# Kernel tuning notes

Measured on AMD Instinct MI355X. Metric: run time of the kernel, lower is better.

Reference implementation:

```python
import jax, jax.numpy as jnp
import numpy as np
from jax import lax

# dims
B, N, K = 8, 1024, 32          # batch, nodes, kNN neighbors
D, H, DH = 256, 8, 32           # node feature width, heads, head dim
TDIM, NB, HID = 16, 32, 128     # time-embed dim, radial basis count, radial MLP hidden
NLAYERS = 3                     # hidden transformer layers
L = NLAYERS + 1                 # + output layer
NS = 128                        # scalar channels sliced into edge attrs
SHD = 9                         # spherical harmonics dim for lmax=2 (1+3+5)
RMAX = 2.0
EIN = NB + TDIM + 2 * NS        # edge-MLP input width


def _sph(u):
    # real spherical harmonics l=0,1,2 with 'component' normalization of unit vec u
    x, y, z = u[..., 0], u[..., 1], u[..., 2]
    l0 = jnp.ones_like(x)[..., None]
    l1 = np.sqrt(3.0) * u
    l2 = jnp.stack([
        np.sqrt(15.0) * x * y,
        np.sqrt(15.0) * y * z,
        0.5 * np.sqrt(5.0) * (3.0 * z * z - 1.0),
        np.sqrt(15.0) * x * z,
        0.5 * np.sqrt(15.0) * (x * x - y * y),
    ], -1)
    return jnp.concatenate([l0, l1, l2], -1)


def _rbf(r):
    # e3nn soft_one_hot_linspace(basis='gaussian', cutoff=False) * sqrt(NB) * 0.95
    centers = jnp.linspace(0.0, RMAX, NB)
    step = RMAX / (NB - 1)
    e = jnp.exp(-((r[..., None] - centers) / step) ** 2) / 1.12
    return e * (NB ** 0.5) * 0.95


def _sus(x):
    # e3nn smooth unit step: exp(-1/x) for x>0 else 0
    return jnp.where(x > 0, jnp.exp(-1.0 / jnp.where(x > 0, x, 1.0)), 0.0)


def setup_inputs() -> dict:
    key = jax.random.key(0)
    ks = jax.random.split(key, 12)
    g = lambda k, shape, fan: (jax.random.normal(k, shape, jnp.float32) / np.sqrt(fan))
    return {
        'x': jax.random.normal(ks[0], (B, N, 3), jnp.float32),
        'y': jax.random.normal(ks[1], (B, N, 3), jnp.float32),
        't': jax.random.uniform(ks[2], (B, TDIM), jnp.float32),
        'W_embed': g(ks[3], (3 + TDIM, D), 3 + TDIM),
        'Wk1': g(ks[4], (L, EIN, HID), EIN),
        'bk1': jnp.zeros((L, HID), jnp.float32),
        'Wk2': g(ks[5], (L, HID, H * DH), HID),
        'Wq': g(ks[6], (L, D, H * DH), D),
        'Wv': g(ks[7], (L, D + SHD, H * DH), D + SHD),
        'Wo': g(ks[8], (NLAYERS, H * DH, D), H * DH),
        'Wo_out': g(ks[9], (H * DH, 3), H * DH),
    }


def _forward(x, y, t, W_embed, Wk1, bk1, Wk2, Wq, Wv, Wo, Wo_out):
    def score(pos, feat, tt):
        # kNN graph: full pairwise distance + top_k (self included, as in source)
        d2 = jnp.sum((pos[:, None, :] - pos[None, :, :]) ** 2, -1)      # [N,N]
        src = lax.top_k(-d2, K)[1]                                       # [N,K], dst = row index
        vec = pos[:, None, :] - pos[src]                                 # pos[dst]-pos[src], [N,K,3]
        r = jnp.linalg.norm(vec, axis=-1)                                # [N,K]
        u = vec / jnp.maximum(r[..., None], 1e-9)
        sh = _sph(u)                                                     # [N,K,SHD]
        cut = 1.4 * _sus(10.0 * (1.0 - r / RMAX))                        # [N,K]
        rbf = _rbf(r) * cut[..., None]                                   # [N,K,NB]
        t_nodes = jnp.broadcast_to(tt, (N, TDIM))
        edge_base = jnp.concatenate([rbf, jnp.broadcast_to(tt, (N, K, TDIM))], -1)
        node = jnp.concatenate([feat, t_nodes], -1) @ W_embed            # [N,D]
        for l in range(L):
            # gather scalar node channels onto edges
            e = jnp.concatenate([edge_base, node[src][..., :NS],
                                 jnp.broadcast_to(node[:, None, :NS], (N, K, NS))], -1)  # [N,K,EIN]
            h = jax.nn.gelu(e @ Wk1[l] + bk1[l])                          # radial MLP
            kf = (h @ Wk2[l]).reshape(N, K, H, DH)
            q = (node @ Wq[l]).reshape(N, H, DH)
            logits = jnp.einsum('nhd,nkhd->nkh', q, kf) / np.sqrt(DH)
            # cutoff-weighted softmax over neighbors (e3nn Transformer style)
            w = cut[..., None] * jnp.exp(logits - logits.max(1, keepdims=True))
            alpha = w / (w.sum(1, keepdims=True) + 1e-9)                  # [N,K,H]
            v = (jnp.concatenate([node[src], sh], -1) @ Wv[l]).reshape(N, K, H, DH)
            agg = jnp.einsum('nkh,nkhd->nhd', alpha, v).reshape(N, H * DH)
            if l < NLAYERS:
                node = node + agg @ Wo[l]                                  # residual
                # scalar activation: gelu on 0e, tanh on 0o, identity on higher l
                node = jnp.concatenate([jax.nn.gelu(node[:, :64]),
                                        jnp.tanh(node[:, 64:NS]),
                                        node[:, NS:]], -1)
            else:
                node = agg @ Wo_out                                        # project to 1x1e
        return node  # [N,3]

    return jax.vmap(score)(x, y, t)


def reference(x, y, t, W_embed, Wk1, bk1, Wk2, Wq, Wv, Wo, Wo_out):
    return _forward(x, y, t, W_embed, Wk1, bk1, Wk2, Wq, Wv, Wo, Wo_out)
```

## Files before the change

kernel.cpp:

```cpp
#include <hip/hip_runtime.h>
#include <math.h>

#define Bb 8
#define Nn 1024
#define Kk 32
#define Dd 256
#define Hh 8
#define DHh 32
#define TDIMt 16
#define NBnb 32
#define HIDh 128
#define NSns 128
#define SHDs 9
#define EINe 304
#define NCOLS 1536

typedef __bf16 bf16_t;
typedef bf16_t bf16x8 __attribute__((ext_vector_type(8)));
typedef float floatx4 __attribute__((ext_vector_type(4)));

#define GLOAD_LDS16(gp, lp) __builtin_amdgcn_global_load_lds( \
    (const __attribute__((address_space(1))) void*)(gp),      \
    (__attribute__((address_space(3))) void*)(lp), 16, 0, 0)

__device__ __forceinline__ float gelu_fast(float x){
  float g = 1.5957691216057308f*(x + 0.044715f*x*x*x);
  return x*__builtin_amdgcn_rcpf(1.0f + __expf(-g));
}
__device__ __forceinline__ float tanh_fast(float x){
  return 1.0f - 2.0f*__builtin_amdgcn_rcpf(1.0f + __expf(2.0f*x));
}

__global__ __launch_bounds__(256) void setup_kernel(
    const float* __restrict__ x, const float* __restrict__ y, const float* __restrict__ t,
    const float* __restrict__ We, const float* __restrict__ Wk1, const float* __restrict__ bk1,
    const float* __restrict__ Wk2, const float* __restrict__ Wq, const float* __restrict__ Wv,
    const float* __restrict__ Wo,
    bf16_t* __restrict__ Wt, bf16_t* __restrict__ Wto, bf16_t* __restrict__ WrbfT,
    float* __restrict__ t_hd, int* __restrict__ src,
    float* __restrict__ node, bf16_t* __restrict__ node_bf){

  __shared__ float s_b[32];
  __shared__ unsigned long long s_knn[4][64];
  const int bid = blockIdx.x, tid = threadIdx.x;

  if (bid < 2048){
    int wave = tid >> 6, lane = tid & 63;
    int bn = bid*4 + wave;
    int b = bn >> 10, n = bn & (Nn-1);
    const float* xb = x + (size_t)b*Nn*3;
    float px = xb[n*3+0], py = xb[n*3+1], pz = xb[n*3+2];
    float d2v[16];
    #pragma unroll
    for (int i=0;i<16;i++){
      int j = i*64 + lane;
      float dx = px - xb[j*3+0];
      float dy = py - xb[j*3+1];
      float dz = pz - xb[j*3+2];
      d2v[i] = dx*dx + dy*dy + dz*dz;
    }

    unsigned lob = 0u, hib = 0x7149F2CAu;
    float T = 1.0f;
    int lc = 0;
    for (int it=0; it<24; ++it){
      lc = 0;
      #pragma unroll
      for (int i=0;i<16;i++) lc += (d2v[i] <= T) ? 1 : 0;
      int c = lc;
      #pragma unroll
      for (int off=32; off>=1; off>>=1) c += __shfl_xor(c, off);
      if (c >= 32 && c <= 64) break;
      if (c < 32) lob = __float_as_uint(T); else hib = __float_as_uint(T);
      float ratio = 44.0f * __builtin_amdgcn_rcpf((float)(c < 1 ? 1 : c));
      float Tn = T * __powf(ratio, 0.6666667f);
      unsigned tb = __float_as_uint(Tn);
      if (tb <= lob || tb >= hib) tb = lob + ((hib - lob) >> 1);
      T = __uint_as_float(tb);
    }

    int pre = lc;
    #pragma unroll
    for (int d=1; d<64; d<<=1){
      int o = __shfl_up(pre, d);
      if (lane >= d) pre += o;
    }
    int wo = pre - lc;

    unsigned long long* sl = s_knn[wave];
    sl[lane] = ~0ull;
    #pragma unroll
    for (int i=0;i<16;i++){
      if (d2v[i] <= T && wo < 64){
        sl[wo] = (((unsigned long long)__float_as_uint(d2v[i])) << 10)
                 | (unsigned)(i*64 + lane);
        wo++;
      }
    }
    __syncthreads();

    unsigned long long key = sl[lane];
    #pragma unroll
    for (int k2=2; k2<=64; k2<<=1){
      #pragma unroll
      for (int j2=k2>>1; j2>=1; j2>>=1){
        unsigned long long pv = __shfl_xor(key, j2);
        bool takeMin = (((lane & j2) == 0) == ((lane & k2) == 0));
        bool pLess = pv < key;
        key = (pLess == takeMin) ? pv : key;
      }
    }
    if (lane < 32) src[(size_t)bn*Kk + lane] = (int)(key & 1023u);
  } else if (bid < 6144){
    int i = bid-2048; int l = i>>10, yy = i&1023;
    int h = yy>>7, c = yy&127;
    if (tid < 32) s_b[tid] = Wk2[(size_t)l*HIDh*Dd + (size_t)c*Dd + h*DHh + tid];
    __syncthreads();
    const int rloc = tid>>3, dg = tid&7;
    const float b0 = s_b[dg*4+0], b1 = s_b[dg*4+1], b2 = s_b[dg*4+2], b3 = s_b[dg*4+3];
    #pragma unroll
    for (int p=0;p<8;p++){
      int ii = p*32 + rloc;
      const float4 v = *(const float4*)(Wq + (size_t)l*Dd*Dd + (size_t)ii*Dd + h*DHh + dg*4);
      float part = v.x*b0 + v.y*b1 + v.z*b2 + v.w*b3;
      part += __shfl_xor(part, 1);
      part += __shfl_xor(part, 2);
      part += __shfl_xor(part, 4);
      if (dg == 0) Wt[((size_t)l*NCOLS + 512 + yy)*Dd + ii] = (bf16_t)part;
    }
  } else if (bid < 8192){
    int i = bid-6144; int l = i>>9, c = i&511, k = tid;
    const float* wk1l = Wk1 + (size_t)l*EINe*HIDh;
    float v;
    if (c < 256)       v = Wv[(size_t)l*265*Dd + (size_t)k*Dd + c];
    else if (c < 384){ int c2 = c-256; v = (k < 128) ? wk1l[(48+k)*HIDh + c2] : 0.0f; }
    else             { int c2 = c-384; v = (k < 128) ? wk1l[(176+k)*HIDh + c2] : 0.0f; }
    Wt[((size_t)l*NCOLS + c)*Dd + k] = (bf16_t)v;
  } else if (bid < 8960){
    int i = bid-8192; int l = i>>8; int c = i&255; int k = tid;
    Wto[((size_t)l*Dd + c)*Dd + k] = (bf16_t)Wo[(size_t)l*Dd*Dd + (size_t)k*Dd + c];
  } else if (bid < 9024){
    int i = bid-8960; int l = i>>4, cg = i&15;
    int c = cg*8 + (tid>>5), k = tid&31;
    WrbfT[((size_t)l*HIDh + c)*NBnb + k] = (bf16_t)Wk1[(size_t)l*EINe*HIDh + (size_t)k*HIDh + c];
  } else if (bid < 9040){
    int i = bid-9024; int pair = i*2 + (tid>>7);
    int l = pair>>3, b = pair&7, c = tid&127;
    const float* wk1l = Wk1 + (size_t)l*EINe*HIDh;
    float a = bk1[l*HIDh + c];
    #pragma unroll
    for (int ii=0;ii<TDIMt;ii++) a += t[b*TDIMt+ii]*wk1l[(32+ii)*HIDh + c];
    t_hd[(l*Bb + b)*HIDh + c] = a;
  } else {
    int bn0 = (bid-9040)*4; int c = tid;
    float w0 = We[0*Dd+c], w1 = We[1*Dd+c], w2 = We[2*Dd+c];
    float wt[TDIMt];
    #pragma unroll
    for (int i=0;i<TDIMt;i++) wt[i] = We[(3+i)*Dd+c];
    #pragma unroll
    for (int u=0;u<4;u++){
      int bn = bn0 + u; int b = bn >> 10;
      float a = y[(size_t)bn*3+0]*w0 + y[(size_t)bn*3+1]*w1 + y[(size_t)bn*3+2]*w2;
      #pragma unroll
      for (int i=0;i<TDIMt;i++) a += t[b*TDIMt+i]*wt[i];
      node[(size_t)bn*Dd + c] = a;
      node_bf[(size_t)bn*Dd + c] = (bf16_t)a;
    }
  }
}

__global__ __launch_bounds__(256) void gemm_proj(const bf16_t* __restrict__ A,
    const bf16_t* __restrict__ Wt_all, float* __restrict__ vproj_f,
    bf16_t* __restrict__ hsrc_bf, float* __restrict__ hdst_f,
    bf16_t* __restrict__ qw_bf, const float* __restrict__ t_hd, int layer){

  __shared__ __align__(16) bf16_t s_A[2][8192];
  __shared__ __align__(16) bf16_t s_B[2][4096];

  const int tid = threadIdx.x;
  const int wave = tid>>6, lane = tid&63;
  const int row16 = lane&15, quad = lane>>4;
  const int bx = blockIdx.x;
  const int brow = ((bx & 7) << 3) + (bx >> 3);
  const int m0 = brow*128;
  const int m_base = m0 + wave*32;
  const int n_base = blockIdx.y*64;
  const bf16_t* Ab = A + (size_t)m0*Dd;
  const bf16_t* Bw = Wt_all + ((size_t)layer*NCOLS + n_base)*Dd;

  const int trow = tid>>3;
  const int tk   = ((tid&7) ^ (trow&7)) << 3;
  const int swz  = (row16&7) << 3;

  floatx4 acc[2][4];
  #pragma unroll
  for (int mi=0;mi<2;mi++)
    #pragma unroll
    for (int ni=0;ni<4;ni++){ floatx4 z = {0.f,0.f,0.f,0.f}; acc[mi][ni] = z; }

  {
    const bf16_t* ga = Ab + (size_t)trow*Dd + tk;
    #pragma unroll
    for (int i=0;i<4;i++) GLOAD_LDS16(ga + (size_t)i*32*Dd, &s_A[0][i*2048 + tid*8]);
    const bf16_t* gb = Bw + (size_t)trow*Dd + tk;
    #pragma unroll
    for (int j=0;j<2;j++) GLOAD_LDS16(gb + (size_t)j*32*Dd, &s_B[0][j*2048 + tid*8]);
  }
  __syncthreads();

  #pragma unroll
  for (int kt=0; kt<4; kt++){
    const int cur = kt&1, nxt = cur^1;
    if (kt < 3){
      const bf16_t* ga = Ab + (size_t)trow*Dd + (kt+1)*64 + tk;
      #pragma unroll
      for (int i=0;i<4;i++) GLOAD_LDS16(ga + (size_t)i*32*Dd, &s_A[nxt][i*2048 + tid*8]);
      const bf16_t* gb = Bw + (size_t)trow*Dd + (kt+1)*64 + tk;
      #pragma unroll
      for (int j=0;j<2;j++) GLOAD_LDS16(gb + (size_t)j*32*Dd, &s_B[nxt][j*2048 + tid*8]);
    }
    #pragma unroll
    for (int ksub=0; ksub<2; ksub++){
      const int ko = (ksub*32 + quad*8) ^ swz;
      bf16x8 a0 = *(const bf16x8*)&s_A[cur][(wave*32      + row16)*64 + ko];
      bf16x8 a1 = *(const bf16x8*)&s_A[cur][(wave*32 + 16 + row16)*64 + ko];
      #pragma unroll
      for (int ni=0;ni<4;ni++){
        bf16x8 b = *(const bf16x8*)&s_B[cur][(ni*16 + row16)*64 + ko];
        acc[0][ni] = __builtin_amdgcn_mfma_f32_16x16x32_bf16(a0, b, acc[0][ni], 0,0,0);
        acc[1][ni] = __builtin_amdgcn_mfma_f32_16x16x32_bf16(a1, b, acc[1][ni], 0,0,0);
      }
    }
    __syncthreads();
  }

  const int by = blockIdx.y;
  const int bb = m_base >> 10;
  #pragma unroll
  for (int mi=0;mi<2;mi++)
    #pragma unroll
    for (int ni=0;ni<4;ni++){
      int col = n_base + ni*16 + row16;
      #pragma unroll
      for (int r=0;r<4;r++){
        int row = m_base + mi*16 + quad*4 + r;
        float v = acc[mi][ni][r];
        if (by < 4)       vproj_f[(size_t)row*256 + col]        = v;
        else if (by < 6)  hsrc_bf[(size_t)row*128 + (col-256)]  = (bf16_t)v;
        else if (by < 8)  hdst_f[(size_t)row*128 + (col-384)]   = v + t_hd[(size_t)(layer*Bb + bb)*HIDh + (col-384)];
        else              qw_bf[(size_t)row*1024 + (col-512)]   = (bf16_t)v;
      }
    }
}

__global__ __launch_bounds__(256) void gemm_upd(
    const bf16_t* __restrict__ agg_bf, const bf16_t* __restrict__ Wto,
    const float* __restrict__ node_in, float* __restrict__ node_out,
    bf16_t* __restrict__ node_bf, int lu, int write_node){

  __shared__ __align__(16) bf16_t s_A[2][8192];
  __shared__ __align__(16) bf16_t s_B[2][4096];

  const int tid = threadIdx.x;
  const int wave = tid>>6, lane = tid&63;
  const int row16 = lane&15, quad = lane>>4;
  const int bx = blockIdx.x;
  const int brow = ((bx & 7) << 3) + (bx >> 3);
  const int m0 = brow*128;
  const int m_base = m0 + wave*32;
  const int n_base = blockIdx.y*64;
  const bf16_t* Ab = agg_bf + (size_t)m0*Dd;
  const bf16_t* Bw = Wto + (size_t)lu*Dd*Dd + (size_t)n_base*Dd;

  const int trow = tid>>3;
  const int tk   = ((tid&7) ^ (trow&7)) << 3;
  const int swz  = (row16&7) << 3;

  floatx4 acc[2][4];
  #pragma unroll
  for (int mi=0;mi<2;mi++)
    #pragma unroll
    for (int ni=0;ni<4;ni++){ floatx4 z = {0.f,0.f,0.f,0.f}; acc[mi][ni] = z; }

  {
    const bf16_t* ga = Ab + (size_t)trow*Dd + tk;
    #pragma unroll
    for (int i=0;i<4;i++) GLOAD_LDS16(ga + (size_t)i*32*Dd, &s_A[0][i*2048 + tid*8]);
    const bf16_t* gb = Bw + (size_t)trow*Dd + tk;
    #pragma unroll
    for (int j=0;j<2;j++) GLOAD_LDS16(gb + (size_t)j*32*Dd, &s_B[0][j*2048 + tid*8]);
  }
  __syncthreads();

  #pragma unroll
  for (int kt=0; kt<4; kt++){
    const int cur = kt&1, nxt = cur^1;
    if (kt < 3){
      const bf16_t* ga = Ab + (size_t)trow*Dd + (kt+1)*64 + tk;
      #pragma unroll
      for (int i=0;i<4;i++) GLOAD_LDS16(ga + (size_t)i*32*Dd, &s_A[nxt][i*2048 + tid*8]);
      const bf16_t* gb = Bw + (size_t)trow*Dd + (kt+1)*64 + tk;
      #pragma unroll
      for (int j=0;j<2;j++) GLOAD_LDS16(gb + (size_t)j*32*Dd, &s_B[nxt][j*2048 + tid*8]);
    }
    #pragma unroll
    for (int ksub=0; ksub<2; ksub++){
      const int ko = (ksub*32 + quad*8) ^ swz;
      bf16x8 a0 = *(const bf16x8*)&s_A[cur][(wave*32      + row16)*64 + ko];
      bf16x8 a1 = *(const bf16x8*)&s_A[cur][(wave*32 + 16 + row16)*64 + ko];
      #pragma unroll
      for (int ni=0;ni<4;ni++){
        bf16x8 b = *(const bf16x8*)&s_B[cur][(ni*16 + row16)*64 + ko];
        acc[0][ni] = __builtin_amdgcn_mfma_f32_16x16x32_bf16(a0, b, acc[0][ni], 0,0,0);
        acc[1][ni] = __builtin_amdgcn_mfma_f32_16x16x32_bf16(a1, b, acc[1][ni], 0,0,0);
      }
    }
    __syncthreads();
  }

  #pragma unroll
  for (int mi=0;mi<2;mi++)
    #pragma unroll
    for (int ni=0;ni<4;ni++){
      int col = n_base + ni*16 + row16;
      #pragma unroll
      for (int r=0;r<4;r++){
        int row = m_base + mi*16 + quad*4 + r;
        float v = acc[mi][ni][r] + node_in[(size_t)row*Dd + col];
        if (col < 64)       v = gelu_fast(v);
        else if (col < 128) v = tanh_fast(v);
        if (write_node) node_out[(size_t)row*Dd + col] = v;
        node_bf[(size_t)row*Dd + col] = (bf16_t)v;
      }
    }
}

__global__ __launch_bounds__(128) void attn_kernel(
    const float* __restrict__ x, const int* __restrict__ src,
    const float* __restrict__ vproj_f, const bf16_t* __restrict__ hsrc_bf,
    const float* __restrict__ hdst_f, const bf16_t* __restrict__ qw_bf,
    const bf16_t* __restrict__ WrbfT,
    const float* __restrict__ Wvg, const float* __restrict__ Woo,
    bf16_t* __restrict__ agg_bf, float* __restrict__ out, int layer){

  __shared__ __align__(16) char smem[11488];
  bf16_t* s_h     = (bf16_t*)(smem);
  float*  s_part  = (float*)(smem);
  float*  s_sh    = (float*)(smem + 8704);
  float*  s_cut   = (float*)(smem + 9984);
  float*  s_logit = (float*)(smem + 10112);
  float*  s_pool  = (float*)(smem + 11136);
  float*  s_red   = (float*)(smem + 11456);

  const int tid  = threadIdx.x;
  const int bidx = blockIdx.x;
  const int b    = bidx & 7;
  const int bn   = (b << 10) | (bidx >> 3);
  const int wv   = tid>>6, lane = tid&63;
  const int row16 = lane&15, quad = lane>>4;

  bf16x8 qf[4];
  { const bf16_t* qp = qw_bf + (size_t)bn*1024 + row16*HIDh + quad*8;
    #pragma unroll
    for (int ks=0; ks<4; ks++) qf[ks] = *(const bf16x8*)(qp + ks*32); }
  float hdv[4];
  #pragma unroll
  for (int ni=0; ni<4; ni++) hdv[ni] = hdst_f[(size_t)bn*128 + wv*64 + ni*16 + row16];

  const float ax = x[(size_t)bn*3+0], ay = x[(size_t)bn*3+1], az = x[(size_t)bn*3+2];

  const int sE0 = src[(size_t)bn*Kk + row16];
  const int sE1 = src[(size_t)bn*Kk + row16 + 16];

  const int e0 = tid>>3, cg = tid&7;
  const int sG0 = src[(size_t)bn*Kk + e0];
  const int sG1 = src[(size_t)bn*Kk + e0 + 16];
  bf16x8 hsv00 = *(const bf16x8*)(hsrc_bf + ((size_t)b*Nn + sG0)*128 + cg*8);
  bf16x8 hsv01 = *(const bf16x8*)(hsrc_bf + ((size_t)b*Nn + sG0)*128 + cg*8 + 64);
  bf16x8 hsv10 = *(const bf16x8*)(hsrc_bf + ((size_t)b*Nn + sG1)*128 + cg*8);
  bf16x8 hsv11 = *(const bf16x8*)(hsrc_bf + ((size_t)b*Nn + sG1)*128 + cg*8 + 64);

  bf16x8 a0f, a1f;
  {
    const float* xj0 = x + ((size_t)b*Nn + sE0)*3;
    const float* xj1 = x + ((size_t)b*Nn + sE1)*3;
    float d0x = ax - xj0[0], d0y = ay - xj0[1], d0z = az - xj0[2];
    float d1x = ax - xj1[0], d1y = ay - xj1[1], d1z = az - xj1[2];
    float rr0 = sqrtf(d0x*d0x + d0y*d0y + d0z*d0z);
    float rr1 = sqrtf(d1x*d1x + d1y*d1y + d1z*d1z);
    float xx0 = 10.0f*(1.0f - rr0*0.5f);
    float xx1 = 10.0f*(1.0f - rr1*0.5f);
    float cu0 = (xx0 > 0.0f) ? 1.4f*__expf(-__builtin_amdgcn_rcpf(xx0)) : 0.0f;
    float cu1 = (xx1 > 0.0f) ? 1.4f*__expf(-__builtin_amdgcn_rcpf(xx1)) : 0.0f;
    float sc0 = 4.798224586623f*cu0;
    float sc1 = 4.798224586623f*cu1;
    float rs0 = fminf(rr0*15.5f, 33.0f);
    float rs1 = fminf(rr1*15.5f, 33.0f);
    float cbase = (float)(quad*8);
    float dd0 = rs0 - cbase, dd1 = rs1 - cbase;
    float e0v = __expf(-dd0*dd0)*sc0;
    float e1v = __expf(-dd1*dd1)*sc1;
    float g0 = __expf(2.0f*dd0 - 1.0f);
    float g1 = __expf(2.0f*dd1 - 1.0f);
    a0f[0] = (bf16_t)e0v; a1f[0] = (bf16_t)e1v;
    #pragma unroll
    for (int j=1;j<8;j++){
      e0v *= g0; e1v *= g1;
      a0f[j] = (bf16_t)e0v; a1f[j] = (bf16_t)e1v;
      g0 *= 0.13533528323661270f; g1 *= 0.13533528323661270f;
    }
  }

  if (tid < 64){
    const int k = tid & 31;
    const int j = src[(size_t)bn*Kk + k];
    const float* xj = x + ((size_t)b*Nn + j)*3;
    float dx = ax - xj[0], dy = ay - xj[1], dz = az - xj[2];
    float rr = sqrtf(dx*dx + dy*dy + dz*dz);
    if (tid < 32){
      float xx = 10.0f*(1.0f - rr*0.5f);
      s_cut[k] = (xx > 0.0f) ? 1.4f*__expf(-__builtin_amdgcn_rcpf(xx)) : 0.0f;
    } else {
      float inv = __builtin_amdgcn_rcpf(fmaxf(rr, 1e-9f));
      float ux = dx*inv, uy = dy*inv, uz = dz*inv;
      float* sh = s_sh + k*10;
      sh[0] = 1.0f;
      sh[1] = 1.7320508075688772f*ux;
      sh[2] = 1.7320508075688772f*uy;
      sh[3] = 1.7320508075688772f*uz;
      sh[4] = 3.872983346207417f*ux*uy;
      sh[5] = 3.872983346207417f*uy*uz;
      sh[6] = 1.118033988749895f*(3.0f*uz*uz - 1.0f);
      sh[7] = 3.872983346207417f*ux*uz;
      sh[8] = 1.9364916731037085f*(ux*ux - uy*uy);
    }
  }

  floatx4 acc[2][4];
  {
    #pragma unroll
    for (int mi=0;mi<2;mi++)
      #pragma unroll
      for (int ni=0;ni<4;ni++){ floatx4 z = {0.f,0.f,0.f,0.f}; acc[mi][ni] = z; }
    const bf16_t* bp = WrbfT + ((size_t)layer*HIDh + wv*64 + row16)*NBnb + quad*8;
    #pragma unroll
    for (int j=0;j<4;j++){
      bf16x8 bbf = *(const bf16x8*)(bp + (size_t)j*16*NBnb);
      acc[0][j] = __builtin_amdgcn_mfma_f32_16x16x32_bf16(a0f, bbf, acc[0][j], 0,0,0);
      acc[1][j] = __builtin_amdgcn_mfma_f32_16x16x32_bf16(a1f, bbf, acc[1][j], 0,0,0);
    }
  }

  *(bf16x8*)(s_h + e0*136 + cg*8)            = hsv00;
  *(bf16x8*)(s_h + e0*136 + cg*8 + 64)       = hsv01;
  *(bf16x8*)(s_h + (e0+16)*136 + cg*8)       = hsv10;
  *(bf16x8*)(s_h + (e0+16)*136 + cg*8 + 64)  = hsv11;
  __syncthreads();

  #pragma unroll
  for (int ni=0;ni<4;ni++){
    int c = wv*64 + ni*16 + row16;
    #pragma unroll
    for (int mi=0;mi<2;mi++){
      #pragma unroll
      for (int r=0;r<4;r++){
        int e = mi*16 + quad*4 + r;
        float hs = (float)s_h[e*136 + c];
        s_h[e*136 + c] = (bf16_t)gelu_fast(acc[mi][ni][r] + hdv[ni] + hs);
      }
    }
  }
  __syncthreads();

  {
    floatx4 la = {0.f,0.f,0.f,0.f};
    #pragma unroll
    for (int ks=0; ks<4; ks++){
      bf16x8 a = *(const bf16x8*)(s_h + (wv*16 + row16)*136 + ks*32 + quad*8);
      la = __builtin_amdgcn_mfma_f32_16x16x32_bf16(a, qf[ks], la, 0,0,0);
    }
    if (row16 < Hh){
      #pragma unroll
      for (int r=0;r<4;r++)
        s_logit[(wv*16 + quad*4 + r)*8 + row16] = la[r]*0.17677669529663687f;
    }
  }
  __syncthreads();

  {
    const int k = tid & 31;
    const int h0 = tid >> 5;
    #pragma unroll
    for (int hh=0; hh<2; hh++){
      const int h = h0 + hh*4;
      float lv = s_logit[k*8 + h];
      float m = lv;
      #pragma unroll
      for (int off=16; off>=1; off>>=1) m = fmaxf(m, __shfl_xor(m, off));
      float w = s_cut[k]*__expf(lv - m);
      float ss = w;
      #pragma unroll
      for (int off=16; off>=1; off>>=1) ss += __shfl_xor(ss, off);
      s_logit[k*8 + h] = w*__builtin_amdgcn_rcpf(ss + 1e-9f);
    }
  }
  __syncthreads();

  {
    const int h2 = tid>>4, sg = tid&15;
    if (sg < SHDs){
      float a = 0.0f;
      #pragma unroll
      for (int k2=0;k2<Kk;k2++)
        a += s_logit[k2*8 + h2] * s_sh[k2*10 + sg];
      s_pool[h2*10 + sg] = a;
    }
  }

  {
    const float* rowp[16];
    #pragma unroll
    for (int i=0;i<16;i++){
      int row = __builtin_amdgcn_readfirstlane(src[(size_t)bn*Kk + wv*16 + i]);
      rowp[i] = vproj_f + ((size_t)b*Nn + row)*256;
    }
    const int albase = wv*128 + (lane>>3);
    float4 accv = {0.f,0.f,0.f,0.f};
    #pragma unroll
    for (int i=0;i<16;i++){
      const float4 v = *(const float4*)(rowp[i] + (lane<<2));
      float al = s_logit[albase + i*8];
      accv.x += al*v.x; accv.y += al*v.y; accv.z += al*v.z; accv.w += al*v.w;
    }
    *(float4*)(s_part + wv*256 + (lane<<2)) = accv;
  }
  __syncthreads();

  {
    const float* wvsh = Wvg + (size_t)layer*265*Dd + 256*Dd;
    float p0 = 0.f, p1 = 0.f, p2 = 0.f;
    #pragma unroll
    for (int cc=0; cc<2; cc++){
      const int c = tid + cc*128;
      const int h = c >> 5;
      float a_main = s_part[c] + s_part[256 + c];
      #pragma unroll
      for (int sg=0; sg<SHDs; sg++) a_main += s_pool[h*10 + sg]*wvsh[sg*Dd + c];

      if (layer < 3){
        agg_bf[(size_t)bn*Dd + c] = (bf16_t)a_main;
      } else {
        p0 += a_main*Woo[c*3+0];
        p1 += a_main*Woo[c*3+1];
        p2 += a_main*Woo[c*3+2];
      }
    }
    if (layer >= 3){
      #pragma unroll
      for (int off=32; off>=1; off>>=1){
        p0 += __shfl_xor(p0, off);
        p1 += __shfl_xor(p1, off);
        p2 += __shfl_xor(p2, off);
      }
      if (lane == 0){ s_red[wv*3+0]=p0; s_red[wv*3+1]=p1; s_red[wv*3+2]=p2; }
      __syncthreads();
      if (tid < 3)
        out[(size_t)bn*3 + tid] = s_red[tid] + s_red[3+tid];
    }
  }
}

extern "C" void kernel_launch(void* const* d_in, const int* in_sizes, int n_in,
                              void* d_out, int out_size, void* d_ws, size_t ws_size,
                              hipStream_t stream){
  const float* x   = (const float*)d_in[0];
  const float* y   = (const float*)d_in[1];
  const float* t   = (const float*)d_in[2];
  const float* We  = (const float*)d_in[3];
  const float* Wk1 = (const float*)d_in[4];
  const float* bk1 = (const float*)d_in[5];
  const float* Wk2 = (const float*)d_in[6];
  const float* Wq  = (const float*)d_in[7];
  const float* Wv  = (const float*)d_in[8];
  const float* Wo  = (const float*)d_in[9];
  const float* Woo = (const float*)d_in[10];
  float* out = (float*)d_out;

  char* ws = (char*)d_ws;
  size_t off = 0;
  auto take = [&](size_t bytes)->char*{ char* p = ws + off; off = (off + bytes + 255) & ~(size_t)255; return p; };

  int*    src      = (int*)   take((size_t)Bb*Nn*Kk*4);
  float*  nodeA    = (float*) take((size_t)Bb*Nn*Dd*4);
  float*  nodeB    = (float*) take((size_t)Bb*Nn*Dd*4);
  bf16_t* node_bf  = (bf16_t*)take((size_t)Bb*Nn*Dd*2);
  bf16_t* agg_bf   = (bf16_t*)take((size_t)Bb*Nn*Dd*2);
  float*  vproj_f  = (float*) take((size_t)Bb*Nn*256*4);
  bf16_t* hsrc_bf  = (bf16_t*)take((size_t)Bb*Nn*128*2);
  float*  hdst_f   = (float*) take((size_t)Bb*Nn*128*4);
  bf16_t* qw_bf    = (bf16_t*)take(((size_t)Bb*Nn*1024 + 2048)*2);
  bf16_t* Wt       = (bf16_t*)take((size_t)4*NCOLS*Dd*2);
  bf16_t* Wto      = (bf16_t*)take((size_t)3*Dd*Dd*2);
  bf16_t* WrbfT    = (bf16_t*)take((size_t)4*HIDh*NBnb*2);
  float*  t_hd     = (float*) take((size_t)4*Bb*HIDh*4);

  setup_kernel<<<dim3(11088), 256, 0, stream>>>(x, y, t, We, Wk1, bk1, Wk2, Wq, Wv, Wo,
                                                Wt, Wto, WrbfT, t_hd, src, nodeA, node_bf);

  gemm_proj<<<dim3(64,24), 256, 0, stream>>>(node_bf, Wt, vproj_f, hsrc_bf, hdst_f, qw_bf, t_hd, 0);
  attn_kernel<<<dim3(Bb*Nn), 128, 0, stream>>>(x, src, vproj_f, hsrc_bf, hdst_f, qw_bf,
                                               WrbfT, Wv, Woo, agg_bf, out, 0);
  const float* nin[3]  = {nodeA, nodeB, nodeA};
  float*       nout[3] = {nodeB, nodeA, nodeB};
  for (int l=1; l<4; l++){
    gemm_upd<<<dim3(64,4), 256, 0, stream>>>(agg_bf, Wto, nin[l-1], nout[l-1], node_bf,
                                             l-1, (l < 3) ? 1 : 0);
    gemm_proj<<<dim3(64,24), 256, 0, stream>>>(node_bf, Wt, vproj_f, hsrc_bf, hdst_f, qw_bf, t_hd, l);
    attn_kernel<<<dim3(Bb*Nn), 128, 0, stream>>>(x, src, vproj_f, hsrc_bf, hdst_f, qw_bf,
                                                 WrbfT, Wv, Woo, agg_bf, out, l);
  }
}
```

Measured before the change: 399.0 us.

## Restructure attention kernel to one wave per node, four nodes per block

```diff
diff --git a/kernel.cpp b/kernel.cpp
--- a/kernel.cpp
+++ b/kernel.cpp
@@ -17,6 +17,7 @@
 
 typedef __bf16 bf16_t;
 typedef bf16_t bf16x8 __attribute__((ext_vector_type(8)));
+typedef bf16_t bf16x4v __attribute__((ext_vector_type(4)));
 typedef float floatx4 __attribute__((ext_vector_type(4)));
 
 #define GLOAD_LDS16(gp, lp) __builtin_amdgcn_global_load_lds( \
@@ -335,7 +336,7 @@
     }
 }
 
-__global__ __launch_bounds__(128) void attn_kernel(
+__global__ __launch_bounds__(256) void attn_kernel(
     const float* __restrict__ x, const int* __restrict__ src,
     const float* __restrict__ vproj_f, const bf16_t* __restrict__ hsrc_bf,
     const float* __restrict__ hdst_f, const bf16_t* __restrict__ qw_bf,
@@ -343,43 +344,42 @@
     const float* __restrict__ Wvg, const float* __restrict__ Woo,
     bf16_t* __restrict__ agg_bf, float* __restrict__ out, int layer){
 
-  __shared__ __align__(16) char smem[11488];
-  bf16_t* s_h     = (bf16_t*)(smem);
-  float*  s_part  = (float*)(smem);
-  float*  s_sh    = (float*)(smem + 8704);
-  float*  s_cut   = (float*)(smem + 9984);
-  float*  s_logit = (float*)(smem + 10112);
-  float*  s_pool  = (float*)(smem + 11136);
-  float*  s_red   = (float*)(smem + 11456);
-
+  __shared__ __align__(16) char smem[46080];
   const int tid  = threadIdx.x;
+  const int wave = tid>>6, lane = tid&63;
+  char* sw = smem + wave*11520;
+  bf16_t* s_h   = (bf16_t*)(sw);
+  float*  s_al  = (float*)(sw + 8704);
+  float*  s_sh  = (float*)(sw + 9728);
+  float*  s_cut = (float*)(sw + 11008);
+  float*  s_pool= (float*)(sw + 11136);
+
   const int bidx = blockIdx.x;
   const int b    = bidx & 7;
-  const int bn   = (b << 10) | (bidx >> 3);
-  const int wv   = tid>>6, lane = tid&63;
+  const int bn   = (b << 10) | ((bidx >> 3) << 2) | wave;
   const int row16 = lane&15, quad = lane>>4;
 
   bf16x8 qf[4];
   { const bf16_t* qp = qw_bf + (size_t)bn*1024 + row16*HIDh + quad*8;
     #pragma unroll
     for (int ks=0; ks<4; ks++) qf[ks] = *(const bf16x8*)(qp + ks*32); }
-  float hdv[4];
-  #pragma unroll
-  for (int ni=0; ni<4; ni++) hdv[ni] = hdst_f[(size_t)bn*128 + wv*64 + ni*16 + row16];
+  float hdv[8];
+  #pragma unroll
+  for (int j=0; j<8; j++) hdv[j] = hdst_f[(size_t)bn*128 + j*16 + row16];
 
   const float ax = x[(size_t)bn*3+0], ay = x[(size_t)bn*3+1], az = x[(size_t)bn*3+2];
+
+  bf16x8 hsv[8];
+  {
+    const int eg = lane>>1, half = lane&1;
+    const int sG = src[(size_t)bn*Kk + eg];
+    const bf16_t* hp = hsrc_bf + ((size_t)b*Nn + sG)*128 + half*64;
+    #pragma unroll
+    for (int j=0;j<8;j++) hsv[j] = *(const bf16x8*)(hp + j*8);
+  }
 
   const int sE0 = src[(size_t)bn*Kk + row16];
   const int sE1 = src[(size_t)bn*Kk + row16 + 16];
-
-  const int e0 = tid>>3, cg = tid&7;
-  const int sG0 = src[(size_t)bn*Kk + e0];
-  const int sG1 = src[(size_t)bn*Kk + e0 + 16];
-  bf16x8 hsv00 = *(const bf16x8*)(hsrc_bf + ((size_t)b*Nn + sG0)*128 + cg*8);
-  bf16x8 hsv01 = *(const bf16x8*)(hsrc_bf + ((size_t)b*Nn + sG0)*128 + cg*8 + 64);
-  bf16x8 hsv10 = *(const bf16x8*)(hsrc_bf + ((size_t)b*Nn + sG1)*128 + cg*8);
-  bf16x8 hsv11 = *(const bf16x8*)(hsrc_bf + ((size_t)b*Nn + sG1)*128 + cg*8 + 64);
-
   bf16x8 a0f, a1f;
   {
     const float* xj0 = x + ((size_t)b*Nn + sE0)*3;
@@ -411,13 +411,13 @@
     }
   }
 
-  if (tid < 64){
-    const int k = tid & 31;
+  {
+    const int k = lane & 31;
     const int j = src[(size_t)bn*Kk + k];
     const float* xj = x + ((size_t)b*Nn + j)*3;
     float dx = ax - xj[0], dy = ay - xj[1], dz = az - xj[2];
     float rr = sqrtf(dx*dx + dy*dy + dz*dz);
-    if (tid < 32){
+    if (lane < 32){
       float xx = 10.0f*(1.0f - rr*0.5f);
       s_cut[k] = (xx > 0.0f) ? 1.4f*__expf(-__builtin_amdgcn_rcpf(xx)) : 0.0f;
     } else {
@@ -436,136 +436,151 @@
     }
   }
 
-  floatx4 acc[2][4];
-  {
-    #pragma unroll
-    for (int mi=0;mi<2;mi++)
-      #pragma unroll
-      for (int ni=0;ni<4;ni++){ floatx4 z = {0.f,0.f,0.f,0.f}; acc[mi][ni] = z; }
-    const bf16_t* bp = WrbfT + ((size_t)layer*HIDh + wv*64 + row16)*NBnb + quad*8;
-    #pragma unroll
-    for (int j=0;j<4;j++){
+  floatx4 acc0[8], acc1[8];
+  {
+    const bf16_t* bp = WrbfT + ((size_t)layer*HIDh + row16)*NBnb + quad*8;
+    #pragma unroll
+    for (int j=0;j<8;j++){
+      floatx4 z = {0.f,0.f,0.f,0.f};
       bf16x8 bbf = *(const bf16x8*)(bp + (size_t)j*16*NBnb);
-      acc[0][j] = __builtin_amdgcn_mfma_f32_16x16x32_bf16(a0f, bbf, acc[0][j], 0,0,0);
-      acc[1][j] = __builtin_amdgcn_mfma_f32_16x16x32_bf16(a1f, bbf, acc[1][j], 0,0,0);
-    }
-  }
-
-  *(bf16x8*)(s_h + e0*136 + cg*8)            = hsv00;
-  *(bf16x8*)(s_h + e0*136 + cg*8 + 64)       = hsv01;
-  *(bf16x8*)(s_h + (e0+16)*136 + cg*8)       = hsv10;
-  *(bf16x8*)(s_h + (e0+16)*136 + cg*8 + 64)  = hsv11;
-  __syncthreads();
-
-  #pragma unroll
-  for (int ni=0;ni<4;ni++){
-    int c = wv*64 + ni*16 + row16;
-    #pragma unroll
-    for (int mi=0;mi<2;mi++){
+      acc0[j] = __builtin_amdgcn_mfma_f32_16x16x32_bf16(a0f, bbf, z, 0,0,0);
+      acc1[j] = __builtin_amdgcn_mfma_f32_16x16x32_bf16(a1f, bbf, z, 0,0,0);
+    }
+  }
+
+  {
+    const int eg = lane>>1, half = lane&1;
+    #pragma unroll
+    for (int j=0;j<8;j++)
+      *(bf16x8*)(s_h + eg*136 + half*64 + j*8) = hsv[j];
+  }
+
+  #pragma unroll
+  for (int j=0;j<8;j++){
+    const int c = j*16 + row16;
+    const float hd = hdv[j];
+    #pragma unroll
+    for (int r=0;r<4;r++){
+      int e = quad*4 + r;
+      float hs = (float)s_h[e*136 + c];
+      s_h[e*136 + c] = (bf16_t)gelu_fast(acc0[j][r] + hd + hs);
+    }
+    #pragma unroll
+    for (int r=0;r<4;r++){
+      int e = 16 + quad*4 + r;
+      float hs = (float)s_h[e*136 + c];
+      s_h[e*136 + c] = (bf16_t)gelu_fast(acc1[j][r] + hd + hs);
+    }
+  }
+
+  floatx4 la[2];
+  #pragma unroll
+  for (int rg=0; rg<2; rg++){
+    floatx4 l4 = {0.f,0.f,0.f,0.f};
+    #pragma unroll
+    for (int ks=0; ks<4; ks++){
+      bf16x8 a = *(const bf16x8*)(s_h + (rg*16 + row16)*136 + ks*32 + quad*8);
+      l4 = __builtin_amdgcn_mfma_f32_16x16x32_bf16(a, qf[ks], l4, 0,0,0);
+    }
+    la[rg] = l4;
+  }
+
+  {
+    float lv[8], ct[8];
+    #pragma unroll
+    for (int rg=0; rg<2; rg++)
       #pragma unroll
       for (int r=0;r<4;r++){
-        int e = mi*16 + quad*4 + r;
-        float hs = (float)s_h[e*136 + c];
-        s_h[e*136 + c] = (bf16_t)gelu_fast(acc[mi][ni][r] + hdv[ni] + hs);
-      }
-    }
-  }
-  __syncthreads();
-
-  {
-    floatx4 la = {0.f,0.f,0.f,0.f};
-    #pragma unroll
-    for (int ks=0; ks<4; ks++){
-      bf16x8 a = *(const bf16x8*)(s_h + (wv*16 + row16)*136 + ks*32 + quad*8);
-      la = __builtin_amdgcn_mfma_f32_16x16x32_bf16(a, qf[ks], la, 0,0,0);
-    }
+        lv[rg*4+r] = la[rg][r]*0.17677669529663687f;
+        ct[rg*4+r] = s_cut[rg*16 + quad*4 + r];
+      }
+    float m = lv[0];
+    #pragma unroll
+    for (int i=1;i<8;i++) m = fmaxf(m, lv[i]);
+    m = fmaxf(m, __shfl_xor(m, 16));
+    m = fmaxf(m, __shfl_xor(m, 32));
+    float w[8]; float ss = 0.f;
+    #pragma unroll
+    for (int i=0;i<8;i++){ w[i] = ct[i]*__expf(lv[i]-m); ss += w[i]; }
+    ss += __shfl_xor(ss, 16);
+    ss += __shfl_xor(ss, 32);
+    float rs = __builtin_amdgcn_rcpf(ss + 1e-9f);
     if (row16 < Hh){
       #pragma unroll
-      for (int r=0;r<4;r++)
-        s_logit[(wv*16 + quad*4 + r)*8 + row16] = la[r]*0.17677669529663687f;
-    }
-  }
-  __syncthreads();
-
-  {
-    const int k = tid & 31;
-    const int h0 = tid >> 5;
-    #pragma unroll
-    for (int hh=0; hh<2; hh++){
-      const int h = h0 + hh*4;
-      float lv = s_logit[k*8 + h];
-      float m = lv;
-      #pragma unroll
-      for (int off=16; off>=1; off>>=1) m = fmaxf(m, __shfl_xor(m, off));
-      float w = s_cut[k]*__expf(lv - m);
-      float ss = w;
-      #pragma unroll
-      for (int off=16; off>=1; off>>=1) ss += __shfl_xor(ss, off);
-      s_logit[k*8 + h] = w*__builtin_amdgcn_rcpf(ss + 1e-9f);
-    }
-  }
-  __syncthreads();
-
-  {
-    const int h2 = tid>>4, sg = tid&15;
-    if (sg < SHDs){
-      float a = 0.0f;
+      for (int rg=0; rg<2; rg++)
+        #pragma unroll
+        for (int r=0;r<4;r++)
+          s_al[(rg*16 + quad*4 + r)*8 + row16] = w[rg*4+r]*rs;
+    }
+  }
+
+  {
+    const int h2 = lane>>3, sg = lane&7;
+    float a = 0.0f;
+    #pragma unroll
+    for (int k2=0;k2<Kk;k2++)
+      a += s_al[k2*8 + h2] * s_sh[k2*10 + sg];
+    s_pool[h2*10 + sg] = a;
+    if (lane < 8){
+      float a8 = 0.0f;
       #pragma unroll
       for (int k2=0;k2<Kk;k2++)
-        a += s_logit[k2*8 + h2] * s_sh[k2*10 + sg];
-      s_pool[h2*10 + sg] = a;
-    }
-  }
-
-  {
-    const float* rowp[16];
-    #pragma unroll
-    for (int i=0;i<16;i++){
-      int row = __builtin_amdgcn_readfirstlane(src[(size_t)bn*Kk + wv*16 + i]);
-      rowp[i] = vproj_f + ((size_t)b*Nn + row)*256;
-    }
-    const int albase = wv*128 + (lane>>3);
-    float4 accv = {0.f,0.f,0.f,0.f};
-    #pragma unroll
-    for (int i=0;i<16;i++){
-      const float4 v = *(const float4*)(rowp[i] + (lane<<2));
-      float al = s_logit[albase + i*8];
-      accv.x += al*v.x; accv.y += al*v.y; accv.z += al*v.z; accv.w += al*v.w;
-    }
-    *(float4*)(s_part + wv*256 + (lane<<2)) = accv;
-  }
-  __syncthreads();
-
-  {
+        a8 += s_al[k2*8 + lane] * s_sh[k2*10 + 8];
+      s_pool[lane*10 + 8] = a8;
+    }
+  }
+
+  float4 accv = {0.f,0.f,0.f,0.f};
+  {
+    const int h = lane>>3;
+    #pragma unroll
+    for (int g=0; g<4; g++){
+      const float* rp[8];
+      #pragma unroll
+      for (int i=0;i<8;i++){
+        int row = __builtin_amdgcn_readfirstlane(src[(size_t)bn*Kk + g*8 + i]);
+        rp[i] = vproj_f + ((size_t)b*Nn + row)*256;
+      }
+      #pragma unroll
+      for (int i=0;i<8;i++){
+        const float4 v = *(const float4*)(rp[i] + (lane<<2));
+        float al = s_al[(g*8+i)*8 + h];
+        accv.x += al*v.x; accv.y += al*v.y; accv.z += al*v.z; accv.w += al*v.w;
+      }
+    }
+  }
+
+  {
+    const int h = lane>>3;
     const float* wvsh = Wvg + (size_t)layer*265*Dd + 256*Dd;
-    float p0 = 0.f, p1 = 0.f, p2 = 0.f;
-    #pragma unroll
-    for (int cc=0; cc<2; cc++){
-      const int c = tid + cc*128;
-      const int h = c >> 5;
-      float a_main = s_part[c] + s_part[256 + c];
-      #pragma unroll
-      for (int sg=0; sg<SHDs; sg++) a_main += s_pool[h*10 + sg]*wvsh[sg*Dd + c];
-
-      if (layer < 3){
-        agg_bf[(size_t)bn*Dd + c] = (bf16_t)a_main;
-      } else {
-        p0 += a_main*Woo[c*3+0];
-        p1 += a_main*Woo[c*3+1];
-        p2 += a_main*Woo[c*3+2];
-      }
-    }
-    if (layer >= 3){
+    #pragma unroll
+    for (int sg=0; sg<SHDs; sg++){
+      const float4 wv4 = *(const float4*)(wvsh + sg*Dd + (lane<<2));
+      const float pl = s_pool[h*10 + sg];
+      accv.x += pl*wv4.x; accv.y += pl*wv4.y; accv.z += pl*wv4.z; accv.w += pl*wv4.w;
+    }
+
+    if (layer < 3){
+      bf16x4v o;
+      o[0] = (bf16_t)accv.x; o[1] = (bf16_t)accv.y;
+      o[2] = (bf16_t)accv.z; o[3] = (bf16_t)accv.w;
+      *(bf16x4v*)(agg_bf + (size_t)bn*Dd + (lane<<2)) = o;
+    } else {
+      const int c0 = lane<<2;
+      float p0 = accv.x*Woo[c0*3+0] + accv.y*Woo[c0*3+3] + accv.z*Woo[c0*3+6] + accv.w*Woo[c0*3+9];
+      float p1 = accv.x*Woo[c0*3+1] + accv.y*Woo[c0*3+4] + accv.z*Woo[c0*3+7] + accv.w*Woo[c0*3+10];
+      float p2 = accv.x*Woo[c0*3+2] + accv.y*Woo[c0*3+5] + accv.z*Woo[c0*3+8] + accv.w*Woo[c0*3+11];
       #pragma unroll
       for (int off=32; off>=1; off>>=1){
         p0 += __shfl_xor(p0, off);
         p1 += __shfl_xor(p1, off);
         p2 += __shfl_xor(p2, off);
       }
-      if (lane == 0){ s_red[wv*3+0]=p0; s_red[wv*3+1]=p1; s_red[wv*3+2]=p2; }
-      __syncthreads();
-      if (tid < 3)
-        out[(size_t)bn*3 + tid] = s_red[tid] + s_red[3+tid];
+      if (lane == 0){
+        out[(size_t)bn*3+0] = p0;
+        out[(size_t)bn*3+1] = p1;
+        out[(size_t)bn*3+2] = p2;
+      }
     }
   }
 }
@@ -608,15 +623,15 @@
                                                 Wt, Wto, WrbfT, t_hd, src, nodeA, node_bf);
 
   gemm_proj<<<dim3(64,24), 256, 0, stream>>>(node_bf, Wt, vproj_f, hsrc_bf, hdst_f, qw_bf, t_hd, 0);
-  attn_kernel<<<dim3(Bb*Nn), 128, 0, stream>>>(x, src, vproj_f, hsrc_bf, hdst_f, qw_bf,
-                                               WrbfT, Wv, Woo, agg_bf, out, 0);
+  attn_kernel<<<dim3(Bb*Nn/4), 256, 0, stream>>>(x, src, vproj_f, hsrc_bf, hdst_f, qw_bf,
+                                                 WrbfT, Wv, Woo, agg_bf, out, 0);
   const float* nin[3]  = {nodeA, nodeB, nodeA};
   float*       nout[3] = {nodeB, nodeA, nodeB};
   for (int l=1; l<4; l++){
     gemm_upd<<<dim3(64,4), 256, 0, stream>>>(agg_bf, Wto, nin[l-1], nout[l-1], node_bf,
                                              l-1, (l < 3) ? 1 : 0);
     gemm_proj<<<dim3(64,24), 256, 0, stream>>>(node_bf, Wt, vproj_f, hsrc_bf, hdst_f, qw_bf, t_hd, l);
-    attn_kernel<<<dim3(Bb*Nn), 128, 0, stream>>>(x, src, vproj_f, hsrc_bf, hdst_f, qw_bf,
-                                                 WrbfT, Wv, Woo, agg_bf, out, l);
+    attn_kernel<<<dim3(Bb*Nn/4), 256, 0, stream>>>(x, src, vproj_f, hsrc_bf, hdst_f, qw_bf,
+                                                   WrbfT, Wv, Woo, agg_bf, out, l);
   }
 }
```

After: 383.6 us. -3.8%, faster.
